# Optimization experiments

Measured on AMD Instinct MI355X. Metric: run time of the kernel, lower is better.

## Reference

```python
import jax, jax.numpy as jnp
import numpy as np

B, S, E, H = 2, 2048, 1024, 16
D = E // H  # head_dim = 64


def setup_inputs() -> dict:
    key = jax.random.key(0)
    ks = jax.random.split(key, 6)
    sc = 1.0 / np.sqrt(D)
    return {
        "x": jax.random.normal(ks[0], (B, S, E), dtype=jnp.float32),
        "Wq": jax.random.normal(ks[1], (D, D), dtype=jnp.float32) * sc,
        "Wk": jax.random.normal(ks[2], (D, D), dtype=jnp.float32) * sc,
        "Wv": jax.random.normal(ks[3], (D, D), dtype=jnp.float32) * sc,
        "Wo": jax.random.normal(ks[4], (E, E), dtype=jnp.float32) * (1.0 / np.sqrt(E)),
        "bo": jnp.zeros((E,), dtype=jnp.float32),
    }


def reference(x, Wq, Wk, Wv, Wo, bo):
    b, s, e = x.shape
    # split into heads: (B, H, S, D)
    xh = x.reshape(b, s, H, D).transpose(0, 2, 1, 3)
    # per-head linear projections (weights SHARED across heads); torch Linear: x @ W^T
    q = jnp.einsum('bhsd,ed->bhse', xh, Wq)
    k = jnp.einsum('bhsd,ed->bhse', xh, Wk)
    v = jnp.einsum('bhsd,ed->bhse', xh, Wv)
    # full attention matrix (B, H, S, S) — faithful to the naive original
    energy = jnp.einsum('bhqd,bhkd->bhqk', q, k)
    attn = jax.nn.softmax(energy / jnp.sqrt(jnp.asarray(D, x.dtype)), axis=-1)
    out = jnp.einsum('bhqk,bhkd->bhqd', attn, v)
    out = out.transpose(0, 2, 1, 3).reshape(b, s, e)
    return out @ Wo.T + bo
```

## Files before the change

### kernel.cpp

```cpp
#include <hip/hip_runtime.h>
#include <hip/hip_bf16.h>

#define B 2
#define S 2048
#define E 1024
#define H 16
#define D 64

typedef unsigned short ushort_t;
typedef __attribute__((ext_vector_type(8))) short bf16x8;
typedef __attribute__((ext_vector_type(4))) float f32x4;

static __device__ __forceinline__ ushort_t f2bf(float f) {
    union { float f; unsigned u; } v; v.f = f;
    unsigned r = v.u + 0x7fffu + ((v.u >> 16) & 1u);
    return (ushort_t)(r >> 16);
}

#define MFMA(a, b, c) __builtin_amdgcn_mfma_f32_16x16x32_bf16((a), (b), (c), 0, 0, 0)

__global__ __launch_bounds__(256) void cvt_w(
    const float* __restrict__ Wq, const float* __restrict__ Wk, const float* __restrict__ Wv,
    const float* __restrict__ Wo,
    ushort_t* __restrict__ wqb, ushort_t* __restrict__ wkb, ushort_t* __restrict__ wvb,
    ushort_t* __restrict__ wob)
{
    int gid = blockIdx.x, t = threadIdx.x;
    if (gid < 1024) {
        int i = gid * 1024 + t * 4;
        float4 f = *(const float4*)(Wo + i);
        ushort4 u; u.x = f2bf(f.x); u.y = f2bf(f.y); u.z = f2bf(f.z); u.w = f2bf(f.w);
        *(ushort4*)(wob + i) = u;
    } else {
        int idx = (gid - 1024) * 1024 + t * 4;
        int which = idx >> 12, off = idx & 4095;
        const float* src = (which == 0) ? Wq : (which == 1) ? Wk : Wv;
        ushort_t* dst    = (which == 0) ? wqb : (which == 1) ? wkb : wvb;
        float sc = (which == 0) ? 0.18033688011112042f : 1.0f;
        float4 f = *(const float4*)(src + off);
        ushort4 u; u.x = f2bf(f.x * sc); u.y = f2bf(f.y * sc);
        u.z = f2bf(f.z * sc); u.w = f2bf(f.w * sc);
        *(ushort4*)(dst + off) = u;
    }
}

__global__ __launch_bounds__(256) void qkv_proj(
    const float* __restrict__ x,
    const ushort_t* __restrict__ wq, const ushort_t* __restrict__ wk, const ushort_t* __restrict__ wv,
    ushort_t* __restrict__ q, ushort_t* __restrict__ k, ushort_t* __restrict__ vT)
{
    __shared__ ushort_t Xs[64][72];
    __shared__ ushort_t Wqs[64][72], Wks[64][72], Wvs[64][72];
    int t = threadIdx.x;
    int bh = blockIdx.y, b = bh >> 4, h = bh & 15;
    int s0 = blockIdx.x * 64;

    {
        int i = t >> 2, d0 = (t & 3) * 16;
        const float* xp = x + ((size_t)(b * S + s0 + i)) * E + h * D + d0;
        #pragma unroll
        for (int c = 0; c < 16; c += 4) {
            float4 f = *(const float4*)(xp + c);
            Xs[i][d0 + c + 0] = f2bf(f.x); Xs[i][d0 + c + 1] = f2bf(f.y);
            Xs[i][d0 + c + 2] = f2bf(f.z); Xs[i][d0 + c + 3] = f2bf(f.w);
        }
    }
    {
        int e = t >> 2, d0 = (t & 3) * 16;
        *(bf16x8*)&Wqs[e][d0]     = *(const bf16x8*)(wq + e * 64 + d0);
        *(bf16x8*)&Wqs[e][d0 + 8] = *(const bf16x8*)(wq + e * 64 + d0 + 8);
        *(bf16x8*)&Wks[e][d0]     = *(const bf16x8*)(wk + e * 64 + d0);
        *(bf16x8*)&Wks[e][d0 + 8] = *(const bf16x8*)(wk + e * 64 + d0 + 8);
        *(bf16x8*)&Wvs[e][d0]     = *(const bf16x8*)(wv + e * 64 + d0);
        *(bf16x8*)&Wvs[e][d0 + 8] = *(const bf16x8*)(wv + e * 64 + d0 + 8);
    }
    __syncthreads();

    int w = t >> 6, lane = t & 63, m = lane & 15, quad = lane >> 4;
    bf16x8 a0 = *(bf16x8*)&Xs[16 * w + m][quad * 8];
    bf16x8 a1 = *(bf16x8*)&Xs[16 * w + m][32 + quad * 8];
    f32x4 cq[4], ck[4], cv[4];
    #pragma unroll
    for (int nt = 0; nt < 4; nt++) { cq[nt] = (f32x4)0.f; ck[nt] = (f32x4)0.f; cv[nt] = (f32x4)0.f; }
    #pragma unroll
    for (int nt = 0; nt < 4; nt++) {
        bf16x8 b0, b1;
        b0 = *(bf16x8*)&Wqs[nt * 16 + m][quad * 8]; b1 = *(bf16x8*)&Wqs[nt * 16 + m][32 + quad * 8];
        cq[nt] = MFMA(a0, b0, cq[nt]); cq[nt] = MFMA(a1, b1, cq[nt]);
        b0 = *(bf16x8*)&Wks[nt * 16 + m][quad * 8]; b1 = *(bf16x8*)&Wks[nt * 16 + m][32 + quad * 8];
        ck[nt] = MFMA(a0, b0, ck[nt]); ck[nt] = MFMA(a1, b1, ck[nt]);
        b0 = *(bf16x8*)&Wvs[nt * 16 + m][quad * 8]; b1 = *(bf16x8*)&Wvs[nt * 16 + m][32 + quad * 8];
        cv[nt] = MFMA(a0, b0, cv[nt]); cv[nt] = MFMA(a1, b1, cv[nt]);
    }
    size_t base = (size_t)bh * S + s0;
    #pragma unroll
    for (int nt = 0; nt < 4; nt++)
        #pragma unroll
        for (int r = 0; r < 4; r++) {
            size_t idx = (base + 16 * w + quad * 4 + r) * D + nt * 16 + m;
            q[idx] = f2bf(cq[nt][r]);
            k[idx] = f2bf(ck[nt][r]);
        }
    __syncthreads();
    #pragma unroll
    for (int nt = 0; nt < 4; nt++)
        #pragma unroll
        for (int r = 0; r < 4; r++)
            Wvs[nt * 16 + m][16 * w + quad * 4 + r] = f2bf(cv[nt][r]);
    __syncthreads();
    {
        int d0 = t >> 2, sc = (t & 3) * 16;
        ushort_t* vp = vT + ((size_t)bh * D + d0) * S + s0 + sc;
        *(bf16x8*)(vp)     = *(bf16x8*)&Wvs[d0][sc];
        *(bf16x8*)(vp + 8) = *(bf16x8*)&Wvs[d0][sc + 8];
    }
}

__global__ __launch_bounds__(256) void flash_attn(
    const ushort_t* __restrict__ q, const ushort_t* __restrict__ k,
    const ushort_t* __restrict__ vT, ushort_t* __restrict__ ao)
{
    __shared__ ushort_t Ks[64][72];
    __shared__ ushort_t Vt[64][72];
    __shared__ ushort_t Ps[128][72];
    int t = threadIdx.x;
    int bh = blockIdx.y, b = bh >> 4, h = bh & 15;
    int q0 = blockIdx.x * 128;
    int w = t >> 6, lane = t & 63, m = lane & 15, quad = lane >> 4;

    const ushort_t* qb = q + ((size_t)bh * S + q0) * D;
    const ushort_t* kb = k + (size_t)bh * S * D;
    const ushort_t* vb = vT + (size_t)bh * D * S;

    bf16x8 qf[2][2];
    #pragma unroll
    for (int u = 0; u < 2; u++) {
        const ushort_t* qp = qb + (size_t)(w * 32 + u * 16 + m) * D;
        qf[u][0] = *(const bf16x8*)(qp + quad * 8);
        qf[u][1] = *(const bf16x8*)(qp + 32 + quad * 8);
    }

    f32x4 o_[2][4];
    float lsum[2] = {0.f, 0.f};
    #pragma unroll
    for (int u = 0; u < 2; u++)
        #pragma unroll
        for (int dt = 0; dt < 4; dt++) o_[u][dt] = (f32x4)0.f;

    int sr = t >> 2, scc = (t & 3) * 16;

    for (int k0 = 0; k0 < S; k0 += 64) {
        __syncthreads();
        {
            const ushort_t* kp = kb + (size_t)(k0 + sr) * D + scc;
            *(bf16x8*)&Ks[sr][scc]     = *(const bf16x8*)(kp);
            *(bf16x8*)&Ks[sr][scc + 8] = *(const bf16x8*)(kp + 8);
            const ushort_t* vp = vb + (size_t)sr * S + k0 + scc;
            *(bf16x8*)&Vt[sr][scc]     = *(const bf16x8*)(vp);
            *(bf16x8*)&Vt[sr][scc + 8] = *(const bf16x8*)(vp + 8);
        }
        __syncthreads();

        #pragma unroll
        for (int nt = 0; nt < 4; nt++) {
            bf16x8 kf0 = *(bf16x8*)&Ks[nt * 16 + m][quad * 8];
            bf16x8 kf1 = *(bf16x8*)&Ks[nt * 16 + m][32 + quad * 8];
            #pragma unroll
            for (int u = 0; u < 2; u++) {
                f32x4 c = (f32x4)0.f;
                c = MFMA(kf0, qf[u][0], c);
                c = MFMA(kf1, qf[u][1], c);
                unsigned pu[4];
                #pragma unroll
                for (int r = 0; r < 4; r++) {
                    float p = __builtin_amdgcn_exp2f(c[r]);
                    unsigned pt = __float_as_uint(p) & 0xffff0000u;
                    lsum[u] += __uint_as_float(pt);
                    pu[r] = pt;
                }
                unsigned pk0 = __builtin_amdgcn_perm(pu[1], pu[0], 0x07060302u);
                unsigned pk1 = __builtin_amdgcn_perm(pu[3], pu[2], 0x07060302u);
                int ql = w * 32 + u * 16 + m, cc = nt * 16 + quad * 4;
                *(unsigned*)&Ps[ql][cc]     = pk0;
                *(unsigned*)&Ps[ql][cc + 2] = pk1;
            }
        }
        asm volatile("s_waitcnt lgkmcnt(0)" ::: "memory");

        bf16x8 pa[2][2];
        #pragma unroll
        for (int u = 0; u < 2; u++) {
            int ql = w * 32 + u * 16 + m;
            pa[u][0] = *(bf16x8*)&Ps[ql][quad * 8];
            pa[u][1] = *(bf16x8*)&Ps[ql][32 + quad * 8];
        }
        #pragma unroll
        for (int dt = 0; dt < 4; dt++) {
            bf16x8 vf0 = *(bf16x8*)&Vt[dt * 16 + m][quad * 8];
            bf16x8 vf1 = *(bf16x8*)&Vt[dt * 16 + m][32 + quad * 8];
            #pragma unroll
            for (int u = 0; u < 2; u++) {
                o_[u][dt] = MFMA(pa[u][0], vf0, o_[u][dt]);
                o_[u][dt] = MFMA(pa[u][1], vf1, o_[u][dt]);
            }
        }
    }

    float inv[2][4];
    #pragma unroll
    for (int u = 0; u < 2; u++) {
        float l = lsum[u];
        l += __shfl_xor(l, 16, 64);
        l += __shfl_xor(l, 32, 64);
        #pragma unroll
        for (int r = 0; r < 4; r++)
            inv[u][r] = 1.f / __shfl(l, quad * 4 + r, 64);
    }
    #pragma unroll
    for (int u = 0; u < 2; u++)
        #pragma unroll
        for (int dt = 0; dt < 4; dt++)
            #pragma unroll
            for (int r = 0; r < 4; r++) {
                int srow = q0 + w * 32 + u * 16 + quad * 4 + r;
                ao[((size_t)(b * S + srow)) * E + h * D + dt * 16 + m] = f2bf(o_[u][dt][r] * inv[u][r]);
            }
}

__global__ __launch_bounds__(256) void out_proj(
    const ushort_t* __restrict__ A, const ushort_t* __restrict__ Wob,
    const float* __restrict__ bo, float* __restrict__ Y)
{
    __shared__ ushort_t As[128][72];
    __shared__ ushort_t Ws[64][72];
    int t = threadIdx.x;
    int n0 = blockIdx.x * 64, m0 = blockIdx.y * 128;
    int w = t >> 6, lane = t & 63, m = lane & 15, quad = lane >> 4;
    f32x4 acc[2][4];
    #pragma unroll
    for (int u = 0; u < 2; u++)
        #pragma unroll
        for (int nt = 0; nt < 4; nt++) acc[u][nt] = (f32x4)0.f;

    int ar = t >> 1, ac = (t & 1) * 32;
    int wr = t >> 2, wc = (t & 3) * 16;
    for (int k0 = 0; k0 < E; k0 += 64) {
        __syncthreads();
        {
            const ushort_t* ap = A + (size_t)(m0 + ar) * E + k0 + ac;
            #pragma unroll
            for (int i = 0; i < 4; i++)
                *(bf16x8*)&As[ar][ac + 8 * i] = *(const bf16x8*)(ap + 8 * i);
            const ushort_t* wp = Wob + (size_t)(n0 + wr) * E + k0 + wc;
            *(bf16x8*)&Ws[wr][wc]     = *(const bf16x8*)(wp);
            *(bf16x8*)&Ws[wr][wc + 8] = *(const bf16x8*)(wp + 8);
        }
        __syncthreads();
        #pragma unroll
        for (int h2 = 0; h2 < 2; h2++) {
            bf16x8 af[2];
            af[0] = *(bf16x8*)&As[w * 32 + m][h2 * 32 + quad * 8];
            af[1] = *(bf16x8*)&As[w * 32 + 16 + m][h2 * 32 + quad * 8];
            #pragma unroll
            for (int nt = 0; nt < 4; nt++) {
                bf16x8 bfr = *(bf16x8*)&Ws[nt * 16 + m][h2 * 32 + quad * 8];
                acc[0][nt] = MFMA(af[0], bfr, acc[0][nt]);
                acc[1][nt] = MFMA(af[1], bfr, acc[1][nt]);
            }
        }
    }
    #pragma unroll
    for (int u = 0; u < 2; u++)
        #pragma unroll
        for (int nt = 0; nt < 4; nt++)
            #pragma unroll
            for (int r = 0; r < 4; r++) {
                int row = m0 + w * 32 + u * 16 + quad * 4 + r;
                int col = n0 + nt * 16 + m;
                Y[(size_t)row * E + col] = acc[u][nt][r] + bo[col];
            }
}

extern "C" void kernel_launch(void* const* d_in, const int* in_sizes, int n_in,
                              void* d_out, int out_size, void* d_ws, size_t ws_size,
                              hipStream_t stream)
{
    const float* x  = (const float*)d_in[0];
    const float* Wq = (const float*)d_in[1];
    const float* Wk = (const float*)d_in[2];
    const float* Wv = (const float*)d_in[3];
    const float* Wo = (const float*)d_in[4];
    const float* bo = (const float*)d_in[5];
    float* Y = (float*)d_out;

    const size_t n = (size_t)B * H * S * D;
    ushort_t* qw  = (ushort_t*)d_ws;
    ushort_t* kw  = qw + n;
    ushort_t* vTw = kw + n;
    ushort_t* ao  = vTw + n;
    ushort_t* wob = ao + n;
    ushort_t* wqb = wob + (size_t)E * E;
    ushort_t* wkb = wqb + D * D;
    ushort_t* wvb = wkb + D * D;

    cvt_w<<<dim3(1024 + 12), 256, 0, stream>>>(Wq, Wk, Wv, Wo, wqb, wkb, wvb, wob);
    qkv_proj<<<dim3(S / 64, B * H), 256, 0, stream>>>(x, wqb, wkb, wvb, qw, kw, vTw);
    flash_attn<<<dim3(S / 128, B * H), 256, 0, stream>>>(qw, kw, vTw, ao);
    out_proj<<<dim3(E / 64, (B * S) / 128), 256, 0, stream>>>(ao, wob, bo, Y);
}
```

Baseline: 168.9 us.

## Load K/V MFMA fragments directly from global memory, dropping LDS staging and barriers

The flash attention loop no longer stages K and V tiles in shared memory with two block barriers per iteration. Each wave now loads its MFMA fragments for K and V straight from global memory (relying on L1/L2 caching, since all four waves read the same data). The P store to LDS is also merged into one 64-bit write. This removes the barrier stalls and LDS round trips, but quadruples global/L1 traffic per block and drops any overlap the cooperative load offered.

```diff
diff --git a/kernel.cpp b/kernel.cpp
--- a/kernel.cpp
+++ b/kernel.cpp
@@ -120,8 +120,6 @@
     const ushort_t* __restrict__ q, const ushort_t* __restrict__ k,
     const ushort_t* __restrict__ vT, ushort_t* __restrict__ ao)
 {
-    __shared__ ushort_t Ks[64][72];
-    __shared__ ushort_t Vt[64][72];
     __shared__ ushort_t Ps[128][72];
     int t = threadIdx.x;
     int bh = blockIdx.y, b = bh >> 4, h = bh & 15;
@@ -147,29 +145,31 @@
         #pragma unroll
         for (int dt = 0; dt < 4; dt++) o_[u][dt] = (f32x4)0.f;
 
-    int sr = t >> 2, scc = (t & 3) * 16;
+    const ushort_t* kfrag = kb + (size_t)m * D + quad * 8;
+    const ushort_t* vfrag = vb + (size_t)m * S + quad * 8;
 
     for (int k0 = 0; k0 < S; k0 += 64) {
-        __syncthreads();
-        {
-            const ushort_t* kp = kb + (size_t)(k0 + sr) * D + scc;
-            *(bf16x8*)&Ks[sr][scc]     = *(const bf16x8*)(kp);
-            *(bf16x8*)&Ks[sr][scc + 8] = *(const bf16x8*)(kp + 8);
-            const ushort_t* vp = vb + (size_t)sr * S + k0 + scc;
-            *(bf16x8*)&Vt[sr][scc]     = *(const bf16x8*)(vp);
-            *(bf16x8*)&Vt[sr][scc + 8] = *(const bf16x8*)(vp + 8);
-        }
-        __syncthreads();
-
+        bf16x8 kf[4][2], vf[4][2];
         #pragma unroll
         for (int nt = 0; nt < 4; nt++) {
-            bf16x8 kf0 = *(bf16x8*)&Ks[nt * 16 + m][quad * 8];
-            bf16x8 kf1 = *(bf16x8*)&Ks[nt * 16 + m][32 + quad * 8];
+            const ushort_t* kp = kfrag + (size_t)(k0 + nt * 16) * D;
+            kf[nt][0] = *(const bf16x8*)(kp);
+            kf[nt][1] = *(const bf16x8*)(kp + 32);
+        }
+        #pragma unroll
+        for (int dt = 0; dt < 4; dt++) {
+            const ushort_t* vp = vfrag + (size_t)(dt * 16) * S + k0;
+            vf[dt][0] = *(const bf16x8*)(vp);
+            vf[dt][1] = *(const bf16x8*)(vp + 32);
+        }
+
+        #pragma unroll
+        for (int nt = 0; nt < 4; nt++) {
             #pragma unroll
             for (int u = 0; u < 2; u++) {
                 f32x4 c = (f32x4)0.f;
-                c = MFMA(kf0, qf[u][0], c);
-                c = MFMA(kf1, qf[u][1], c);
+                c = MFMA(kf[nt][0], qf[u][0], c);
+                c = MFMA(kf[nt][1], qf[u][1], c);
                 unsigned pu[4];
                 #pragma unroll
                 for (int r = 0; r < 4; r++) {
@@ -181,8 +181,7 @@
                 unsigned pk0 = __builtin_amdgcn_perm(pu[1], pu[0], 0x07060302u);
                 unsigned pk1 = __builtin_amdgcn_perm(pu[3], pu[2], 0x07060302u);
                 int ql = w * 32 + u * 16 + m, cc = nt * 16 + quad * 4;
-                *(unsigned*)&Ps[ql][cc]     = pk0;
-                *(unsigned*)&Ps[ql][cc + 2] = pk1;
+                *(uint2*)&Ps[ql][cc] = make_uint2(pk0, pk1);
             }
         }
         asm volatile("s_waitcnt lgkmcnt(0)" ::: "memory");
@@ -195,15 +194,12 @@
             pa[u][1] = *(bf16x8*)&Ps[ql][32 + quad * 8];
         }
         #pragma unroll
-        for (int dt = 0; dt < 4; dt++) {
-            bf16x8 vf0 = *(bf16x8*)&Vt[dt * 16 + m][quad * 8];
-            bf16x8 vf1 = *(bf16x8*)&Vt[dt * 16 + m][32 + quad * 8];
+        for (int dt = 0; dt < 4; dt++)
             #pragma unroll
             for (int u = 0; u < 2; u++) {
-                o_[u][dt] = MFMA(pa[u][0], vf0, o_[u][dt]);
-                o_[u][dt] = MFMA(pa[u][1], vf1, o_[u][dt]);
-            }
-        }
+                o_[u][dt] = MFMA(pa[u][0], vf[dt][0], o_[u][dt]);
+                o_[u][dt] = MFMA(pa[u][1], vf[dt][1], o_[u][dt]);
+            }
     }
 
     float inv[2][4];
```

Result: slower. 222.3 us (+31.6%).

## Double-buffer K/V tiles in LDS with register prefetch two tiles ahead

Applied to the files above, without the earlier changes.

Turns the flash-attention K/V staging into a double-buffered pipeline. The next tile is written to the alternate LDS buffer and the tile after that is prefetched into registers, so global loads overlap compute and one barrier per iteration goes away. It also merges the two 32-bit P stores into a single 64-bit store. In exchange it doubles K/V LDS use and raises register pressure, which may lower occupancy.

```diff
diff --git a/kernel.cpp b/kernel.cpp
--- a/kernel.cpp
+++ b/kernel.cpp
@@ -120,8 +120,8 @@
     const ushort_t* __restrict__ q, const ushort_t* __restrict__ k,
     const ushort_t* __restrict__ vT, ushort_t* __restrict__ ao)
 {
-    __shared__ ushort_t Ks[64][72];
-    __shared__ ushort_t Vt[64][72];
+    __shared__ ushort_t Ks[2][64][72];
+    __shared__ ushort_t Vt[2][64][72];
     __shared__ ushort_t Ps[128][72];
     int t = threadIdx.x;
     int bh = blockIdx.y, b = bh >> 4, h = bh & 15;
@@ -149,22 +149,47 @@
 
     int sr = t >> 2, scc = (t & 3) * 16;
 
-    for (int k0 = 0; k0 < S; k0 += 64) {
-        __syncthreads();
-        {
-            const ushort_t* kp = kb + (size_t)(k0 + sr) * D + scc;
-            *(bf16x8*)&Ks[sr][scc]     = *(const bf16x8*)(kp);
-            *(bf16x8*)&Ks[sr][scc + 8] = *(const bf16x8*)(kp + 8);
-            const ushort_t* vp = vb + (size_t)sr * S + k0 + scc;
-            *(bf16x8*)&Vt[sr][scc]     = *(const bf16x8*)(vp);
-            *(bf16x8*)&Vt[sr][scc + 8] = *(const bf16x8*)(vp + 8);
-        }
-        __syncthreads();
+    bf16x8 kp0, kp1, vp0, vp1;
+
+    {
+        const ushort_t* kp = kb + (size_t)sr * D + scc;
+        const ushort_t* vp = vb + (size_t)sr * S + scc;
+        kp0 = *(const bf16x8*)(kp);     kp1 = *(const bf16x8*)(kp + 8);
+        vp0 = *(const bf16x8*)(vp);     vp1 = *(const bf16x8*)(vp + 8);
+        *(bf16x8*)&Ks[0][sr][scc]     = kp0;
+        *(bf16x8*)&Ks[0][sr][scc + 8] = kp1;
+        *(bf16x8*)&Vt[0][sr][scc]     = vp0;
+        *(bf16x8*)&Vt[0][sr][scc + 8] = vp1;
+    }
+    __syncthreads();
+    {
+        const ushort_t* kp = kb + (size_t)(64 + sr) * D + scc;
+        const ushort_t* vp = vb + (size_t)sr * S + 64 + scc;
+        kp0 = *(const bf16x8*)(kp);     kp1 = *(const bf16x8*)(kp + 8);
+        vp0 = *(const bf16x8*)(vp);     vp1 = *(const bf16x8*)(vp + 8);
+    }
+
+    const int NT = S / 64;
+    for (int it = 0; it < NT; it++) {
+        int p = it & 1;
+        if (it + 1 < NT) {
+            *(bf16x8*)&Ks[1 - p][sr][scc]     = kp0;
+            *(bf16x8*)&Ks[1 - p][sr][scc + 8] = kp1;
+            *(bf16x8*)&Vt[1 - p][sr][scc]     = vp0;
+            *(bf16x8*)&Vt[1 - p][sr][scc + 8] = vp1;
+        }
+        if (it + 2 < NT) {
+            int k0n = (it + 2) * 64;
+            const ushort_t* kp = kb + (size_t)(k0n + sr) * D + scc;
+            const ushort_t* vp = vb + (size_t)sr * S + k0n + scc;
+            kp0 = *(const bf16x8*)(kp);     kp1 = *(const bf16x8*)(kp + 8);
+            vp0 = *(const bf16x8*)(vp);     vp1 = *(const bf16x8*)(vp + 8);
+        }
 
         #pragma unroll
         for (int nt = 0; nt < 4; nt++) {
-            bf16x8 kf0 = *(bf16x8*)&Ks[nt * 16 + m][quad * 8];
-            bf16x8 kf1 = *(bf16x8*)&Ks[nt * 16 + m][32 + quad * 8];
+            bf16x8 kf0 = *(bf16x8*)&Ks[p][nt * 16 + m][quad * 8];
+            bf16x8 kf1 = *(bf16x8*)&Ks[p][nt * 16 + m][32 + quad * 8];
             #pragma unroll
             for (int u = 0; u < 2; u++) {
                 f32x4 c = (f32x4)0.f;
@@ -173,16 +198,15 @@
                 unsigned pu[4];
                 #pragma unroll
                 for (int r = 0; r < 4; r++) {
-                    float p = __builtin_amdgcn_exp2f(c[r]);
-                    unsigned pt = __float_as_uint(p) & 0xffff0000u;
+                    float pv = __builtin_amdgcn_exp2f(c[r]);
+                    unsigned pt = __float_as_uint(pv) & 0xffff0000u;
                     lsum[u] += __uint_as_float(pt);
                     pu[r] = pt;
                 }
                 unsigned pk0 = __builtin_amdgcn_perm(pu[1], pu[0], 0x07060302u);
                 unsigned pk1 = __builtin_amdgcn_perm(pu[3], pu[2], 0x07060302u);
                 int ql = w * 32 + u * 16 + m, cc = nt * 16 + quad * 4;
-                *(unsigned*)&Ps[ql][cc]     = pk0;
-                *(unsigned*)&Ps[ql][cc + 2] = pk1;
+                *(uint2*)&Ps[ql][cc] = make_uint2(pk0, pk1);
             }
         }
         asm volatile("s_waitcnt lgkmcnt(0)" ::: "memory");
@@ -196,14 +220,15 @@
         }
         #pragma unroll
         for (int dt = 0; dt < 4; dt++) {
-            bf16x8 vf0 = *(bf16x8*)&Vt[dt * 16 + m][quad * 8];
-            bf16x8 vf1 = *(bf16x8*)&Vt[dt * 16 + m][32 + quad * 8];
+            bf16x8 vf0 = *(bf16x8*)&Vt[p][dt * 16 + m][quad * 8];
+            bf16x8 vf1 = *(bf16x8*)&Vt[p][dt * 16 + m][32 + quad * 8];
             #pragma unroll
             for (int u = 0; u < 2; u++) {
                 o_[u][dt] = MFMA(pa[u][0], vf0, o_[u][dt]);
                 o_[u][dt] = MFMA(pa[u][1], vf1, o_[u][dt]);
             }
         }
+        __syncthreads();
     }
 
     float inv[2][4];
```

After: 158.7 us. -6.1%, faster.
